# Kernel tuning notes

Hardware: AMD Instinct MI355X
Metric: run time of the kernel (lower is better)

## Reference

```python
import jax, jax.numpy as jnp
import numpy as np

VOCAB = 50000
EDIM = 128
CDIM = 128
B = 512
LEVEL_FACTORS = [4, 4, 3, 3, 2, 1]  # 7 levels total, N = 403968 nodes


def _build_forest():
    """Deterministic random forest: per-level arrays of token, global parent idx, depth, batch id."""
    rng = np.random.default_rng(0)
    level_sizes = [B]
    for f in LEVEL_FACTORS:
        level_sizes.append(level_sizes[-1] * f)
    offsets = np.cumsum([0] + level_sizes)
    tokens = [rng.integers(0, VOCAB, B)]
    parent = [np.zeros(B, np.int64)]          # roots: dummy parent (depth 0 never scattered)
    depth = [np.zeros(B, np.int64)]
    batch_id = [np.arange(B)]
    for d in range(1, len(level_sizes)):
        n = level_sizes[d]
        tokens.append(rng.integers(0, VOCAB, n))
        p_local = rng.integers(0, level_sizes[d - 1], n)
        parent.append(offsets[d - 1] + p_local)
        depth.append(np.full(n, d, np.int64))
        batch_id.append(batch_id[d - 1][p_local])
    cat = lambda xs: np.concatenate(xs).astype(np.int32)
    return cat(tokens), cat(parent), cat(depth), cat(batch_id), len(level_sizes)


def setup_inputs() -> dict:
    key = jax.random.key(0)
    k1, k2, k3 = jax.random.split(key, 3)
    emb_table = jax.random.normal(k1, (VOCAB, EDIM), dtype=jnp.float32) * 0.02
    W = jax.random.normal(k2, (CDIM, EDIM), dtype=jnp.float32) * 0.02
    b = jax.random.normal(k3, (CDIM,), dtype=jnp.float32) * 0.02
    tokens, parent, depth, batch_id, num_levels = _build_forest()
    return {
        "emb_table": emb_table,
        "W": W,
        "b": b,
        "tokens": jnp.asarray(tokens),
        "parent": jnp.asarray(parent),
        "depth": jnp.asarray(depth),
        "batch_id": jnp.asarray(batch_id),
        "num_levels": num_levels,
        "batch_size": B,
    }


def reference(emb_table, W, b, tokens, parent, depth, batch_id, num_levels, batch_size):
    N = tokens.shape[0]
    # per-node base: W_c(embedding(token))  [N, CDIM]
    base = emb_table[tokens] @ W.T + b
    h = base
    # bottom-up subtree sum, level-batched scatter-add (deepest level first)
    for d in range(num_levels - 1, 0, -1):
        contrib = jnp.where((depth == d)[:, None], h, 0.0)
        h = h + jax.ops.segment_sum(contrib, parent, num_segments=N)
    # per-batch elementwise max over all nodes of the tree, clamped at 0
    # (original maxes zero-initialized snapshots over all recursion calls)
    out = jax.ops.segment_max(h, batch_id, num_segments=batch_size)
    return jnp.maximum(out, 0.0)
```

## Files before the change

kernel.cpp:

```cpp
#include <hip/hip_runtime.h>
#include <hip/hip_bf16.h>


using f32x4   = __attribute__((ext_vector_type(4))) float;
using short8  = __attribute__((ext_vector_type(8))) short;
using ushort8 = __attribute__((ext_vector_type(8))) unsigned short;
using float4v = __attribute__((ext_vector_type(4))) float;

#define N_ALL   403968
#define N_NONRT 403456
#define N_PAR   256512
#define OFF3    10752
#define OFF4    35328
#define OFF5    109056
#define OFF6    256512
#define SEG5    108544
#define LEAFSEG 256000
#define ND5     147456
#define NVOCAB  50000
#define CAPW    384
#define D1CAP   24
#define D2CAP   64
#define WEMB_BLOCKS 782

__device__ __forceinline__ short f2bf(float f) {
  union { float f; unsigned u; } v; v.f = f;
  unsigned r = v.u + 0x7fffu + ((v.u >> 16) & 1u);
  return (short)(r >> 16);
}
__device__ __forceinline__ float bf2f(unsigned short u) {
  union { unsigned u; float f; } v; v.u = ((unsigned)u) << 16; return v.f;
}

__global__ __launch_bounds__(256) void prep_k(const float* __restrict__ W,
                                              const float* __restrict__ emb,
                                              const float* __restrict__ bias,
                                              unsigned short* __restrict__ Wemb,
                                              const int* __restrict__ parent,
                                              int* __restrict__ cnt) {
  if (blockIdx.x >= WEMB_BLOCKS) {
    int i = (blockIdx.x - WEMB_BLOCKS) * 256 + threadIdx.x + 512;
    atomicAdd(cnt + parent[i], 1);
    return;
  }
  __shared__ short WBs[16384];
  for (int idx = threadIdx.x; idx < 16384; idx += 256) {
    int j = idx & 7, c16 = (idx >> 3) & 15, g = (idx >> 7) & 3,
        s = (idx >> 9) & 3, t = idx >> 11;
    WBs[idx] = f2bf(W[(t * 16 + c16) * 128 + s * 32 + g * 8 + j]);
  }
  __syncthreads();

  const int tid = threadIdx.x, lane = tid & 63, wv = tid >> 6;
  const int l15 = lane & 15, g = lane >> 4;
  const int nb = blockIdx.x * 64 + wv * 16;

  f32x4 acc[8];
  #pragma unroll
  for (int t = 0; t < 8; ++t) {
    const float bb = bias[t * 16 + l15];
    #pragma unroll
    for (int j = 0; j < 4; ++j) acc[t][j] = bb;
  }
  int vr = nb + l15; if (vr > NVOCAB - 1) vr = NVOCAB - 1;
  const float* erow = emb + (size_t)vr * 128;
  short8 a[4];
  #pragma unroll
  for (int s = 0; s < 4; ++s) {
    float4v f0 = *(const float4v*)(erow + s * 32 + g * 8);
    float4v f1 = *(const float4v*)(erow + s * 32 + g * 8 + 4);
    short8 t;
    t[0] = f2bf(f0[0]); t[1] = f2bf(f0[1]); t[2] = f2bf(f0[2]); t[3] = f2bf(f0[3]);
    t[4] = f2bf(f1[0]); t[5] = f2bf(f1[1]); t[6] = f2bf(f1[2]); t[7] = f2bf(f1[3]);
    a[s] = t;
  }
  #pragma unroll
  for (int t = 0; t < 8; ++t) {
    #pragma unroll
    for (int s = 0; s < 4; ++s) {
      const short8 bfr = *(const short8*)&WBs[((((t * 4 + s) * 4) + g) * 16 + l15) * 8];
      acc[t] = __builtin_amdgcn_mfma_f32_16x16x32_bf16(a[s], bfr, acc[t], 0, 0, 0);
    }
  }
  #pragma unroll
  for (int j = 0; j < 4; ++j) {
    const int r = nb + g * 4 + j;
    if (r < NVOCAB) {
      ushort8 hv;
      #pragma unroll
      for (int t = 0; t < 8; ++t) hv[t] = (unsigned short)f2bf(acc[t][j]);
      *(ushort8*)(Wemb + (size_t)r * 128 + l15 * 8) = hv;
    }
  }
}

__device__ __forceinline__ int block_excl_scan(int v, int* total) {
  int lane = threadIdx.x & 63, wv = threadIdx.x >> 6;
  int x = v;
  #pragma unroll
  for (int d = 1; d < 64; d <<= 1) { int y = __shfl_up(x, d); if (lane >= d) x += y; }
  __shared__ int ws[4];
  if (lane == 63) ws[wv] = x;
  __syncthreads();
  int off = 0;
  for (int w = 0; w < wv; ++w) off += ws[w];
  __syncthreads();
  if (total) { int t = 0; for (int w = 0; w < 4; ++w) t += ws[w]; *total = t; }
  return x + off - v;
}

__global__ __launch_bounds__(256) void scanA(const int* __restrict__ cnt,
                                             int* __restrict__ start,
                                             int* __restrict__ bsum) {
  int i = blockIdx.x * 256 + threadIdx.x;
  int v = cnt[i];
  int tot;
  int ex = block_excl_scan(v, &tot);
  start[i] = ex;
  if (threadIdx.x == 0) bsum[blockIdx.x] = tot;
}

__global__ __launch_bounds__(256) void scanB(int* __restrict__ b, int n) {
  int base = threadIdx.x * 4;
  int v[4];
  #pragma unroll
  for (int q = 0; q < 4; ++q) v[q] = (base + q < n) ? b[base + q] : 0;
  __syncthreads();
  int s = v[0] + v[1] + v[2] + v[3];
  int ex = block_excl_scan(s, nullptr);
  int run = ex;
  #pragma unroll
  for (int q = 0; q < 4; ++q) {
    if (base + q < n) b[base + q] = run;
    run += v[q];
  }
}

__global__ __launch_bounds__(256) void addcopy(int* __restrict__ start,
                                               int* __restrict__ start_mut,
                                               const int* __restrict__ bsum) {
  int i = blockIdx.x * 256 + threadIdx.x;
  int s = start[i] + bsum[blockIdx.x];
  start[i] = s; start_mut[i] = s;
  if (i == 0) start[N_PAR] = N_NONRT;
}

__global__ __launch_bounds__(256) void fill_k(const int* __restrict__ parent,
                                              const int* __restrict__ tokens,
                                              const int* __restrict__ start,
                                              int* __restrict__ start_mut,
                                              int* __restrict__ chlist,
                                              int* __restrict__ tok5s,
                                              int* __restrict__ meta5) {
  int i = blockIdx.x * 256 + threadIdx.x + 512;
  int p = atomicAdd(start_mut + parent[i], 1);
  chlist[p] = (i >= OFF6) ? tokens[i] : i;
  if (i >= OFF5 && i < OFF6) {
    const int s = p - SEG5;
    tok5s[s] = tokens[i];
    const int ls = start[i], lc = start[i + 1] - ls;
    meta5[s] = ((ls - LEAFSEG) << 6) | lc;
  }
}

__global__ __launch_bounds__(256, 8) void d4f_k(
    const unsigned short* __restrict__ Wemb,
    const int*   __restrict__ tokens,
    const int*   __restrict__ start,
    const int*   __restrict__ chlist,
    const int*   __restrict__ tok5s,
    const int*   __restrict__ meta5,
    unsigned short* __restrict__ Hout)
{
  const int chunk = threadIdx.x & 15;
  const int node  = threadIdx.x >> 4;
  const int nd    = blockIdx.x * 16 + node;
  const int gid   = OFF4 + nd;

  float acc[8], mx[8];
  {
    const int tok = tokens[gid];
    const ushort8 b = *(const ushort8*)(Wemb + (size_t)tok * 128 + chunk * 8);
    #pragma unroll
    for (int t = 0; t < 8; ++t) { acc[t] = bf2f(b[t]); mx[t] = 0.0f; }
  }

  const int s5 = start[gid] - SEG5;
  const int e5 = start[gid + 1] - SEG5;
  for (int c = s5; c < e5; ++c) {
    const int tok5 = tok5s[c];
    const int m    = meta5[c];
    const int lb   = LEAFSEG + (m >> 6);
    const int lc   = m & 63;
    const ushort8 r5 = *(const ushort8*)(Wemb + (size_t)tok5 * 128 + chunk * 8);
    float h5[8], lmx[8];
    #pragma unroll
    for (int t = 0; t < 8; ++t) { h5[t] = bf2f(r5[t]); lmx[t] = 0.0f; }
    for (int l = lb; l < lb + lc; ++l) {
      const int tl = chlist[l];
      const ushort8 rl = *(const ushort8*)(Wemb + (size_t)tl * 128 + chunk * 8);
      #pragma unroll
      for (int t = 0; t < 8; ++t) {
        const float hv = bf2f(rl[t]);
        h5[t] += hv;
        lmx[t] = fmaxf(lmx[t], hv);
      }
    }
    #pragma unroll
    for (int t = 0; t < 8; ++t) {
      acc[t] += h5[t];
      mx[t] = fmaxf(mx[t], fmaxf(lmx[t], h5[t]));
    }
  }

  ushort8 hv, mv;
  #pragma unroll
  for (int t = 0; t < 8; ++t) {
    hv[t] = (unsigned short)f2bf(acc[t]);
    mv[t] = (unsigned short)f2bf(fmaxf(mx[t], acc[t]));
  }
  *(ushort8*)(Hout + (size_t)nd * 256 + chunk * 8) = hv;
  *(ushort8*)(Hout + (size_t)nd * 256 + 128 + chunk * 8) = mv;
}

__global__ __launch_bounds__(256, 4) void d3_k(
    const unsigned short* __restrict__ Wemb,
    const int*   __restrict__ tokens,
    const unsigned short* __restrict__ Hin,
    unsigned short*       __restrict__ Hout,
    const int*   __restrict__ start,
    const int*   __restrict__ chlist)
{
  __shared__ int chl[CAPW];
  const int chunk = threadIdx.x & 15;
  const int node  = threadIdx.x >> 4;
  const int nd    = blockIdx.x * 16 + node;
  const int gid   = OFF3 + nd;

  int bcs = start[OFF3 + blockIdx.x * 16];
  const int bce = start[OFF3 + blockIdx.x * 16 + 16];
  const int nw  = bce - bcs;
  bool useLds = (nw <= CAPW);
  if (useLds)
    for (int i = threadIdx.x; i < nw; i += 256)
      chl[i] = chlist[bcs + i] - OFF4;
  __syncthreads();

  float acc[8], mx[8];
  {
    const int tok = tokens[gid];
    const ushort8 b = *(const ushort8*)(Wemb + (size_t)tok * 128 + chunk * 8);
    #pragma unroll
    for (int t = 0; t < 8; ++t) { acc[t] = bf2f(b[t]); mx[t] = 0.0f; }
  }

  int k = start[gid];
  const int e = start[gid + 1];
  for (; k + 2 <= e; k += 2) {
    int c0, c1;
    if (useLds) { c0 = chl[k - bcs]; c1 = chl[k + 1 - bcs]; }
    else        { c0 = chlist[k] - OFF4; c1 = chlist[k + 1] - OFF4; }
    const ushort8 h0 = *(const ushort8*)(Hin + (size_t)c0 * 256 + chunk * 8);
    const ushort8 m0 = *(const ushort8*)(Hin + (size_t)c0 * 256 + 128 + chunk * 8);
    const ushort8 h1 = *(const ushort8*)(Hin + (size_t)c1 * 256 + chunk * 8);
    const ushort8 m1 = *(const ushort8*)(Hin + (size_t)c1 * 256 + 128 + chunk * 8);
    #pragma unroll
    for (int t = 0; t < 8; ++t) {
      acc[t] += bf2f(h0[t]); mx[t] = fmaxf(mx[t], bf2f(m0[t]));
      acc[t] += bf2f(h1[t]); mx[t] = fmaxf(mx[t], bf2f(m1[t]));
    }
  }
  if (k < e) {
    int c0 = useLds ? chl[k - bcs] : chlist[k] - OFF4;
    const ushort8 h0 = *(const ushort8*)(Hin + (size_t)c0 * 256 + chunk * 8);
    const ushort8 m0 = *(const ushort8*)(Hin + (size_t)c0 * 256 + 128 + chunk * 8);
    #pragma unroll
    for (int t = 0; t < 8; ++t) {
      acc[t] += bf2f(h0[t]); mx[t] = fmaxf(mx[t], bf2f(m0[t]));
    }
  }

  ushort8 hv, mv;
  #pragma unroll
  for (int t = 0; t < 8; ++t) {
    hv[t] = (unsigned short)f2bf(acc[t]);
    mv[t] = (unsigned short)f2bf(fmaxf(mx[t], acc[t]));
  }
  *(ushort8*)(Hout + (size_t)nd * 256 + chunk * 8) = hv;
  *(ushort8*)(Hout + (size_t)nd * 256 + 128 + chunk * 8) = mv;
}

__global__ __launch_bounds__(256, 2) void top_k(
    const unsigned short* __restrict__ Wemb,
    const int*   __restrict__ tokens,
    const unsigned short* __restrict__ Hd3,
    float*       __restrict__ outf,
    const int*   __restrict__ start,
    const int*   __restrict__ chlist)
{
  __shared__ int d1id[D1CAP];
  __shared__ int c2[D1CAP];
  __shared__ int d2off[D1CAP + 1];
  __shared__ int d2id[D2CAP];
  __shared__ int n2s;
  __shared__ unsigned short rec2[D2CAP][256];
  __shared__ unsigned short rec1[D1CAP][256];

  const int r   = blockIdx.x;
  const int tid = threadIdx.x;
  const int chunk = tid & 15, grp = tid >> 4;

  const int s1 = start[r];
  int n1 = start[r + 1] - s1; if (n1 > D1CAP) n1 = D1CAP;
  if (tid < n1) {
    const int g1 = chlist[s1 + tid];
    d1id[tid] = g1;
    c2[tid] = start[g1 + 1] - start[g1];
  }
  __syncthreads();
  if (tid == 0) {
    int run = 0;
    for (int i = 0; i < n1; ++i) {
      d2off[i] = run; run += c2[i];
      if (run > D2CAP) run = D2CAP;
    }
    d2off[n1] = run; n2s = run;
  }
  __syncthreads();
  const int n2 = n2s;
  if (tid < n1) {
    const int g1 = d1id[tid];
    const int s = start[g1], o = d2off[tid], cmax = d2off[tid + 1] - o;
    for (int q = 0; q < cmax; ++q) d2id[o + q] = chlist[s + q];
  }
  __syncthreads();

  for (int i = grp; i < n2; i += 16) {
    const int g2 = d2id[i];
    float acc[8], mx[8];
    {
      const ushort8 b = *(const ushort8*)(Wemb + (size_t)tokens[g2] * 128 + chunk * 8);
      #pragma unroll
      for (int t = 0; t < 8; ++t) { acc[t] = bf2f(b[t]); mx[t] = 0.0f; }
    }
    const int e = start[g2 + 1];
    for (int k = start[g2]; k < e; ++k) {
      const int c3 = chlist[k] - OFF3;
      const ushort8 h0 = *(const ushort8*)(Hd3 + (size_t)c3 * 256 + chunk * 8);
      const ushort8 m0 = *(const ushort8*)(Hd3 + (size_t)c3 * 256 + 128 + chunk * 8);
      #pragma unroll
      for (int t = 0; t < 8; ++t) {
        acc[t] += bf2f(h0[t]); mx[t] = fmaxf(mx[t], bf2f(m0[t]));
      }
    }
    #pragma unroll
    for (int t = 0; t < 8; ++t) {
      rec2[i][chunk * 8 + t] = (unsigned short)f2bf(acc[t]);
      rec2[i][128 + chunk * 8 + t] =
          (unsigned short)f2bf(fmaxf(mx[t], acc[t]));
    }
  }
  __syncthreads();

  for (int i = grp; i < n1; i += 16) {
    const int g1 = d1id[i];
    float acc[8], mx[8];
    {
      const ushort8 b = *(const ushort8*)(Wemb + (size_t)tokens[g1] * 128 + chunk * 8);
      #pragma unroll
      for (int t = 0; t < 8; ++t) { acc[t] = bf2f(b[t]); mx[t] = 0.0f; }
    }
    for (int q = d2off[i]; q < d2off[i + 1]; ++q) {
      #pragma unroll
      for (int t = 0; t < 8; ++t) {
        acc[t] += bf2f(rec2[q][chunk * 8 + t]);
        mx[t] = fmaxf(mx[t], bf2f(rec2[q][128 + chunk * 8 + t]));
      }
    }
    #pragma unroll
    for (int t = 0; t < 8; ++t) {
      rec1[i][chunk * 8 + t] = (unsigned short)f2bf(acc[t]);
      rec1[i][128 + chunk * 8 + t] =
          (unsigned short)f2bf(fmaxf(mx[t], acc[t]));
    }
  }
  __syncthreads();

  if (grp == 0) {
    float acc[8], mx[8];
    {
      const ushort8 b = *(const ushort8*)(Wemb + (size_t)tokens[r] * 128 + chunk * 8);
      #pragma unroll
      for (int t = 0; t < 8; ++t) { acc[t] = bf2f(b[t]); mx[t] = 0.0f; }
    }
    for (int i = 0; i < n1; ++i) {
      #pragma unroll
      for (int t = 0; t < 8; ++t) {
        acc[t] += bf2f(rec1[i][chunk * 8 + t]);
        mx[t] = fmaxf(mx[t], bf2f(rec1[i][128 + chunk * 8 + t]));
      }
    }
    #pragma unroll
    for (int t = 0; t < 8; ++t)
      outf[(size_t)r * 128 + t * 16 + chunk] = fmaxf(mx[t], acc[t]);
  }
}

extern "C" void kernel_launch(void* const* d_in, const int* in_sizes, int n_in,
                              void* d_out, int out_size, void* d_ws, size_t ws_size,
                              hipStream_t stream) {
  (void)in_sizes; (void)n_in; (void)out_size; (void)ws_size;

  const float* emb    = (const float*)d_in[0];
  const float* W      = (const float*)d_in[1];
  const float* bias   = (const float*)d_in[2];
  const int*   tokens = (const int*)d_in[3];
  const int*   parent = (const int*)d_in[4];

  char* p = (char*)d_ws;
  unsigned short* bufB  = (unsigned short*)p;
  unsigned short* bufA  = (unsigned short*)(p + 75497472);
  int*   chlist   = (int*)(p + 113246208);
  int*   start    = (int*)(p + 114860032);
  int*   cnt      = (int*)(p + 115886084);
  int*   bsum     = (int*)(p + 116912132);
  unsigned short* Wemb = (unsigned short*)(p + 116949008);
  int*   tok5s    = (int*)(p + 129749008);
  int*   meta5    = (int*)(p + 130338832);

  float* outf = (float*)d_out;

  hipMemsetAsync(cnt, 0, (size_t)N_PAR * 4, stream);
  prep_k<<<WEMB_BLOCKS + N_NONRT / 256, 256, 0, stream>>>(
      W, emb, bias, Wemb, parent, cnt);
  scanA<<<N_PAR / 256, 256, 0, stream>>>(cnt, start, bsum);
  scanB<<<1, 256, 0, stream>>>(bsum, 1002);
  addcopy<<<N_PAR / 256, 256, 0, stream>>>(start, cnt , bsum);
  fill_k<<<N_NONRT / 256, 256, 0, stream>>>(parent, tokens, start,
                                            cnt , chlist,
                                            tok5s, meta5);

  d4f_k<<<73728 / 16, 256, 0, stream>>>(Wemb, tokens, start, chlist,
                                        tok5s, meta5, bufA);
  d3_k<<<24576 / 16, 256, 0, stream>>>(Wemb, tokens, bufA, bufB, start, chlist);
  top_k<<<512, 256, 0, stream>>>(Wemb, tokens, bufB, outf, start, chlist);
}
```

Baseline: 136.4 us.

## Fuse depth-4 subtree evaluation into depth-3 kernel and fold block-sum scan into addcopy

Merges the depth-4 and depth-3 kernels into a single d3f_k. Each depth-3 node now walks its depth-4, depth-5 and leaf descendants directly through new compact tok4s/meta4 arrays, so the bufA intermediate is never written or read back. The separate single-block scanB launch is also removed: each addcopy block sums the preceding block totals itself. The cost is fewer threads in the fused kernel (24576 nodes instead of 73728) with deeper serial loops, plus redundant prefix summing in addcopy.

```diff
diff --git a/kernel.cpp b/kernel.cpp
--- a/kernel.cpp
+++ b/kernel.cpp
@@ -14,11 +14,10 @@
 #define OFF4    35328
 #define OFF5    109056
 #define OFF6    256512
+#define SEG4    34816
 #define SEG5    108544
 #define LEAFSEG 256000
-#define ND5     147456
 #define NVOCAB  50000
-#define CAPW    384
 #define D1CAP   24
 #define D2CAP   64
 #define WEMB_BLOCKS 782
@@ -120,27 +119,22 @@
   if (threadIdx.x == 0) bsum[blockIdx.x] = tot;
 }
 
-__global__ __launch_bounds__(256) void scanB(int* __restrict__ b, int n) {
-  int base = threadIdx.x * 4;
-  int v[4];
-  #pragma unroll
-  for (int q = 0; q < 4; ++q) v[q] = (base + q < n) ? b[base + q] : 0;
-  __syncthreads();
-  int s = v[0] + v[1] + v[2] + v[3];
-  int ex = block_excl_scan(s, nullptr);
-  int run = ex;
-  #pragma unroll
-  for (int q = 0; q < 4; ++q) {
-    if (base + q < n) b[base + q] = run;
-    run += v[q];
-  }
-}
-
 __global__ __launch_bounds__(256) void addcopy(int* __restrict__ start,
                                                int* __restrict__ start_mut,
                                                const int* __restrict__ bsum) {
+  __shared__ int wsum[4];
+  __shared__ int pfx;
+  int partial = 0;
+  for (int j = threadIdx.x; j < blockIdx.x; j += 256) partial += bsum[j];
+  #pragma unroll
+  for (int d = 32; d > 0; d >>= 1) partial += __shfl_down(partial, d);
+  const int lane = threadIdx.x & 63, wv = threadIdx.x >> 6;
+  if (lane == 0) wsum[wv] = partial;
+  __syncthreads();
+  if (threadIdx.x == 0) pfx = wsum[0] + wsum[1] + wsum[2] + wsum[3];
+  __syncthreads();
   int i = blockIdx.x * 256 + threadIdx.x;
-  int s = start[i] + bsum[blockIdx.x];
+  int s = start[i] + pfx;
   start[i] = s; start_mut[i] = s;
   if (i == 0) start[N_PAR] = N_NONRT;
 }
@@ -150,6 +144,8 @@
                                               const int* __restrict__ start,
                                               int* __restrict__ start_mut,
                                               int* __restrict__ chlist,
+                                              int* __restrict__ tok4s,
+                                              int* __restrict__ meta4,
                                               int* __restrict__ tok5s,
                                               int* __restrict__ meta5) {
   int i = blockIdx.x * 256 + threadIdx.x + 512;
@@ -158,16 +154,21 @@
   if (i >= OFF5 && i < OFF6) {
     const int s = p - SEG5;
     tok5s[s] = tokens[i];
-    const int ls = start[i], lc = start[i + 1] - ls;
-    meta5[s] = ((ls - LEAFSEG) << 6) | lc;
-  }
-}
-
-__global__ __launch_bounds__(256, 8) void d4f_k(
+    meta5[s] = ((start[i] - LEAFSEG) << 6) | (start[i + 1] - start[i]);
+  } else if (i >= OFF4 && i < OFF5) {
+    const int s = p - SEG4;
+    tok4s[s] = tokens[i];
+    meta4[s] = ((start[i] - SEG5) << 6) | (start[i + 1] - start[i]);
+  }
+}
+
+__global__ __launch_bounds__(256, 6) void d3f_k(
     const unsigned short* __restrict__ Wemb,
     const int*   __restrict__ tokens,
     const int*   __restrict__ start,
     const int*   __restrict__ chlist,
+    const int*   __restrict__ tok4s,
+    const int*   __restrict__ meta4,
     const int*   __restrict__ tok5s,
     const int*   __restrict__ meta5,
     unsigned short* __restrict__ Hout)
@@ -175,7 +176,7 @@
   const int chunk = threadIdx.x & 15;
   const int node  = threadIdx.x >> 4;
   const int nd    = blockIdx.x * 16 + node;
-  const int gid   = OFF4 + nd;
+  const int gid   = OFF3 + nd;
 
   float acc[8], mx[8];
   {
@@ -185,98 +186,47 @@
     for (int t = 0; t < 8; ++t) { acc[t] = bf2f(b[t]); mx[t] = 0.0f; }
   }
 
-  const int s5 = start[gid] - SEG5;
-  const int e5 = start[gid + 1] - SEG5;
-  for (int c = s5; c < e5; ++c) {
-    const int tok5 = tok5s[c];
-    const int m    = meta5[c];
-    const int lb   = LEAFSEG + (m >> 6);
-    const int lc   = m & 63;
-    const ushort8 r5 = *(const ushort8*)(Wemb + (size_t)tok5 * 128 + chunk * 8);
-    float h5[8], lmx[8];
-    #pragma unroll
-    for (int t = 0; t < 8; ++t) { h5[t] = bf2f(r5[t]); lmx[t] = 0.0f; }
-    for (int l = lb; l < lb + lc; ++l) {
-      const int tl = chlist[l];
-      const ushort8 rl = *(const ushort8*)(Wemb + (size_t)tl * 128 + chunk * 8);
+  const int s4 = start[gid] - SEG4;
+  const int e4 = start[gid + 1] - SEG4;
+  for (int c4 = s4; c4 < e4; ++c4) {
+    const int tok4 = tok4s[c4];
+    const int m4v  = meta4[c4];
+    const int s5   = m4v >> 6;
+    const int n5   = m4v & 63;
+    const ushort8 r4 = *(const ushort8*)(Wemb + (size_t)tok4 * 128 + chunk * 8);
+    float h4[8], m4[8];
+    #pragma unroll
+    for (int t = 0; t < 8; ++t) { h4[t] = bf2f(r4[t]); m4[t] = 0.0f; }
+
+    for (int c5 = s5; c5 < s5 + n5; ++c5) {
+      const int tok5 = tok5s[c5];
+      const int m5v  = meta5[c5];
+      const int lb   = LEAFSEG + (m5v >> 6);
+      const int lc   = m5v & 63;
+      const ushort8 r5 = *(const ushort8*)(Wemb + (size_t)tok5 * 128 + chunk * 8);
+      float h5[8], lmx[8];
+      #pragma unroll
+      for (int t = 0; t < 8; ++t) { h5[t] = bf2f(r5[t]); lmx[t] = 0.0f; }
+      for (int l = lb; l < lb + lc; ++l) {
+        const int tl = chlist[l];
+        const ushort8 rl = *(const ushort8*)(Wemb + (size_t)tl * 128 + chunk * 8);
+        #pragma unroll
+        for (int t = 0; t < 8; ++t) {
+          const float hv = bf2f(rl[t]);
+          h5[t] += hv;
+          lmx[t] = fmaxf(lmx[t], hv);
+        }
+      }
       #pragma unroll
       for (int t = 0; t < 8; ++t) {
-        const float hv = bf2f(rl[t]);
-        h5[t] += hv;
-        lmx[t] = fmaxf(lmx[t], hv);
+        h4[t] += h5[t];
+        m4[t] = fmaxf(m4[t], fmaxf(lmx[t], h5[t]));
       }
     }
     #pragma unroll
     for (int t = 0; t < 8; ++t) {
-      acc[t] += h5[t];
-      mx[t] = fmaxf(mx[t], fmaxf(lmx[t], h5[t]));
-    }
-  }
-
-  ushort8 hv, mv;
-  #pragma unroll
-  for (int t = 0; t < 8; ++t) {
-    hv[t] = (unsigned short)f2bf(acc[t]);
-    mv[t] = (unsigned short)f2bf(fmaxf(mx[t], acc[t]));
-  }
-  *(ushort8*)(Hout + (size_t)nd * 256 + chunk * 8) = hv;
-  *(ushort8*)(Hout + (size_t)nd * 256 + 128 + chunk * 8) = mv;
-}
-
-__global__ __launch_bounds__(256, 4) void d3_k(
-    const unsigned short* __restrict__ Wemb,
-    const int*   __restrict__ tokens,
-    const unsigned short* __restrict__ Hin,
-    unsigned short*       __restrict__ Hout,
-    const int*   __restrict__ start,
-    const int*   __restrict__ chlist)
-{
-  __shared__ int chl[CAPW];
-  const int chunk = threadIdx.x & 15;
-  const int node  = threadIdx.x >> 4;
-  const int nd    = blockIdx.x * 16 + node;
-  const int gid   = OFF3 + nd;
-
-  int bcs = start[OFF3 + blockIdx.x * 16];
-  const int bce = start[OFF3 + blockIdx.x * 16 + 16];
-  const int nw  = bce - bcs;
-  bool useLds = (nw <= CAPW);
-  if (useLds)
-    for (int i = threadIdx.x; i < nw; i += 256)
-      chl[i] = chlist[bcs + i] - OFF4;
-  __syncthreads();
-
-  float acc[8], mx[8];
-  {
-    const int tok = tokens[gid];
-    const ushort8 b = *(const ushort8*)(Wemb + (size_t)tok * 128 + chunk * 8);
-    #pragma unroll
-    for (int t = 0; t < 8; ++t) { acc[t] = bf2f(b[t]); mx[t] = 0.0f; }
-  }
-
-  int k = start[gid];
-  const int e = start[gid + 1];
-  for (; k + 2 <= e; k += 2) {
-    int c0, c1;
-    if (useLds) { c0 = chl[k - bcs]; c1 = chl[k + 1 - bcs]; }
-    else        { c0 = chlist[k] - OFF4; c1 = chlist[k + 1] - OFF4; }
-    const ushort8 h0 = *(const ushort8*)(Hin + (size_t)c0 * 256 + chunk * 8);
-    const ushort8 m0 = *(const ushort8*)(Hin + (size_t)c0 * 256 + 128 + chunk * 8);
-    const ushort8 h1 = *(const ushort8*)(Hin + (size_t)c1 * 256 + chunk * 8);
-    const ushort8 m1 = *(const ushort8*)(Hin + (size_t)c1 * 256 + 128 + chunk * 8);
-    #pragma unroll
-    for (int t = 0; t < 8; ++t) {
-      acc[t] += bf2f(h0[t]); mx[t] = fmaxf(mx[t], bf2f(m0[t]));
-      acc[t] += bf2f(h1[t]); mx[t] = fmaxf(mx[t], bf2f(m1[t]));
-    }
-  }
-  if (k < e) {
-    int c0 = useLds ? chl[k - bcs] : chlist[k] - OFF4;
-    const ushort8 h0 = *(const ushort8*)(Hin + (size_t)c0 * 256 + chunk * 8);
-    const ushort8 m0 = *(const ushort8*)(Hin + (size_t)c0 * 256 + 128 + chunk * 8);
-    #pragma unroll
-    for (int t = 0; t < 8; ++t) {
-      acc[t] += bf2f(h0[t]); mx[t] = fmaxf(mx[t], bf2f(m0[t]));
+      acc[t] += h4[t];
+      mx[t] = fmaxf(mx[t], fmaxf(m4[t], h4[t]));
     }
   }
 
@@ -419,7 +369,6 @@
 
   char* p = (char*)d_ws;
   unsigned short* bufB  = (unsigned short*)p;
-  unsigned short* bufA  = (unsigned short*)(p + 75497472);
   int*   chlist   = (int*)(p + 113246208);
   int*   start    = (int*)(p + 114860032);
   int*   cnt      = (int*)(p + 115886084);
@@ -427,6 +376,8 @@
   unsigned short* Wemb = (unsigned short*)(p + 116949008);
   int*   tok5s    = (int*)(p + 129749008);
   int*   meta5    = (int*)(p + 130338832);
+  int*   tok4s    = (int*)(p + 130928656);
+  int*   meta4    = (int*)(p + 131223568);
 
   float* outf = (float*)d_out;
 
@@ -434,14 +385,12 @@
   prep_k<<<WEMB_BLOCKS + N_NONRT / 256, 256, 0, stream>>>(
       W, emb, bias, Wemb, parent, cnt);
   scanA<<<N_PAR / 256, 256, 0, stream>>>(cnt, start, bsum);
-  scanB<<<1, 256, 0, stream>>>(bsum, 1002);
   addcopy<<<N_PAR / 256, 256, 0, stream>>>(start, cnt , bsum);
   fill_k<<<N_NONRT / 256, 256, 0, stream>>>(parent, tokens, start,
                                             cnt , chlist,
-                                            tok5s, meta5);
-
-  d4f_k<<<73728 / 16, 256, 0, stream>>>(Wemb, tokens, start, chlist,
-                                        tok5s, meta5, bufA);
-  d3_k<<<24576 / 16, 256, 0, stream>>>(Wemb, tokens, bufA, bufB, start, chlist);
+                                            tok4s, meta4, tok5s, meta5);
+
+  d3f_k<<<24576 / 16, 256, 0, stream>>>(Wemb, tokens, start, chlist,
+                                        tok4s, meta4, tok5s, meta5, bufB);
   top_k<<<512, 256, 0, stream>>>(Wemb, tokens, bufB, outf, start, chlist);
 }
```

Measured after the change: 149.2 us. 9.4% more time.
